# Performance work log

Hardware: AMD Instinct MI355X
Metric: run time of the kernel (lower is better)

The kernel has to match this reference:

```python
import jax, jax.numpy as jnp
import numpy as np

NUM_HEADS = 8
KERNEL = 7
LOW_RANK = 4


def setup_inputs() -> dict:
    key = jax.random.key(0)
    ks = jax.random.split(key, 10)
    B, H, W, C = 4, 56, 56, 256
    nh, K, lr = NUM_HEADS, KERNEL, LOW_RANK
    s = 0.02
    return {
        "x": jax.random.normal(ks[0], (B, H, W, C), jnp.float32),
        "Wq": jax.random.normal(ks[1], (C, nh * lr), jnp.float32) * s,
        "bq": jnp.zeros((nh * lr,), jnp.float32),
        "Wk": jax.random.normal(ks[2], (C, nh * lr), jnp.float32) * s,
        "bk": jnp.zeros((nh * lr,), jnp.float32),
        "Wv": jax.random.normal(ks[3], (C, C), jnp.float32) * s,
        "bv": jnp.zeros((C,), jnp.float32),
        "rpb": jax.random.normal(ks[4], (nh, 2 * K - 1, 2 * K - 1), jnp.float32) * s,
        "Wp": jax.random.normal(ks[5], (C, C), jnp.float32) * s,
        "bp": jnp.zeros((C,), jnp.float32),
    }


def reference(x, Wq, bq, Wk, bk, Wv, bv, rpb, Wp, bp):
    B, H, W, C = x.shape
    nh, K, lr = NUM_HEADS, KERNEL, LOW_RANK
    hd = C // nh
    r = K // 2
    scale = hd ** -0.5

    # Projections. Note: the original uses a raw reshape (B,H,W,nh*lr)->(B,nh,H,W,lr),
    # which we replicate exactly (row-major reshape, no permute).
    q = (x @ Wq + bq).reshape(B, nh, H, W, lr) * scale
    k = (x @ Wk + bk).reshape(B, nh, H, W, lr)
    v = (x @ Wv + bv).reshape(B, nh, H, W, hd)

    # NATTEN window start indices (clamped so each query sees exactly K keys per axis).
    start_h = jnp.clip(jnp.arange(H) - r, 0, H - K)  # (H,)
    start_w = jnp.clip(jnp.arange(W) - r, 0, W - K)  # (W,)
    idx_h = start_h[:, None] + jnp.arange(K)[None, :]  # (H, K)
    idx_w = start_w[:, None] + jnp.arange(K)[None, :]  # (W, K)

    # Gather local K/V windows: (B, nh, H, K, W, K, d)
    k_win = k[:, :, idx_h][:, :, :, :, idx_w]
    v_win = v[:, :, idx_h][:, :, :, :, idx_w]

    # Scores: (B, nh, H, W, K, K)
    attn = jnp.einsum('bhijc,bhikjlc->bhijkl', q, k_win)

    # Relative position bias indices: (key_pos - query_pos) + (K-1)
    bi = idx_h - jnp.arange(H)[:, None] + (K - 1)  # (H, K)
    bj = idx_w - jnp.arange(W)[:, None] + (K - 1)  # (W, K)
    bias = rpb[:, bi][:, :, :, bj]                 # (nh, H, K, W, K)
    attn = attn + bias.transpose(0, 1, 3, 2, 4)[None]  # (B, nh, H, W, K, K)

    attn = jax.nn.softmax(attn.reshape(B, nh, H, W, K * K), axis=-1)
    attn = attn.reshape(B, nh, H, W, K, K)

    # Weighted aggregation of V windows: (B, nh, H, W, hd)
    out = jnp.einsum('bhijkl,bhikjld->bhijd', attn, v_win)
    out = out.transpose(0, 2, 3, 1, 4).reshape(B, H, W, C)
    return out @ Wp + bp
```

## Files before the change

kernel.cpp:

```cpp
#include <hip/hip_runtime.h>
#include <hip/hip_bf16.h>

#define BD 4
#define HD_ 56
#define WD 56
#define CD 256
#define NH 8
#define KW 7
#define LR 4
#define HDIM 32
#define MB (HD_*WD)
#define NROWS (BD*MB)
#define QK_PER_B (HD_*WD*32)
#define V_PER_B  (HD_*WD*256)

typedef short short8 __attribute__((ext_vector_type(8)));
typedef float floatx4 __attribute__((ext_vector_type(4)));

static __device__ inline ushort f2bf(float f) {
    __hip_bfloat16 h = __float2bfloat16(f);
    return *(ushort*)&h;
}
static __device__ inline float bf2f(uint h16) {
    union { uint u; float f; } c; c.u = h16 << 16; return c.f;
}
static __device__ inline float bf2f_hi(uint u) {
    union { uint v; float f; } c; c.v = u & 0xffff0000u; return c.f;
}

typedef const __attribute__((address_space(1))) void* gp1_t;
typedef __attribute__((address_space(3))) void* sp3_t;
static __device__ __forceinline__ void glds16(const void* g, void* s) {
    __builtin_amdgcn_global_load_lds((gp1_t)g, (sp3_t)s, 16, 0, 0);
}

__global__ __launch_bounds__(256) void prep_all(
    const float* __restrict__ x,
    const float* __restrict__ Wq, const float* __restrict__ Wk,
    const float* __restrict__ Wv, const float* __restrict__ bq,
    const float* __restrict__ bk, const float* __restrict__ bv,
    const float* __restrict__ Wp,
    ushort* __restrict__ xb, ushort* __restrict__ WpkT,
    ushort* __restrict__ WpT, float* __restrict__ pb)
{
    int idx = blockIdx.x * 256 + threadIdx.x;
    if (idx < 401408) {
        float4 f0 = *(const float4*)&x[idx * 8];
        float4 f1 = *(const float4*)&x[idx * 8 + 4];
        union { ushort h[8]; uint4 u; } p;
        p.h[0] = f2bf(f0.x); p.h[1] = f2bf(f0.y); p.h[2] = f2bf(f0.z); p.h[3] = f2bf(f0.w);
        p.h[4] = f2bf(f1.x); p.h[5] = f2bf(f1.y); p.h[6] = f2bf(f1.z); p.h[7] = f2bf(f1.w);
        *(uint4*)&xb[idx * 8] = p.u;
    } else if (idx < 401408 + 81920) {
        int j = idx - 401408;
        int n = j >> 8, k = j & 255;
        float v;
        if (n < 32)       v = Wq[k * 32 + n];
        else if (n < 64)  v = Wk[k * 32 + (n - 32)];
        else              v = Wv[k * 256 + (n - 64)];
        WpkT[j] = f2bf(v);
    } else if (idx < 401408 + 81920 + 65536) {
        int j = idx - (401408 + 81920);
        int n = j >> 8, k = j & 255;
        WpT[j] = f2bf(Wp[k * 256 + n]);
    } else if (idx < 401408 + 81920 + 65536 + 320) {
        int n = idx - (401408 + 81920 + 65536);
        pb[n] = (n < 32) ? bq[n] : (n < 64) ? bk[n - 32] : bv[n - 64];
    }
}

static __device__ __forceinline__ void gemm_core_128x64(
    const ushort* __restrict__ Ag, const ushort* __restrict__ Bg,
    ushort* As, ushort* Bs, int m0, int n0, int t, floatx4 (&acc)[4][2])
{
    const int lane = t & 63, w = t >> 6;
    const int lx = lane & 7, ly = lane >> 3;
    const int koff = (lx ^ ly) << 3;
    const int col = lane & 15, quad = lane >> 4;
    const int swz = (col & 7) << 4;
    const int wm = w >> 1, wn = w & 1;
    char* Ac = (char*)As;
    char* Bc = (char*)Bs;

    for (int k0 = 0; k0 < 256; k0 += 64) {
        __syncthreads();
#pragma unroll
        for (int l = 0; l < 4; ++l) {
            int c = (w << 2) + l;
            int row = (c << 3) + ly;
            glds16(&Ag[(m0 + row) * 256 + k0 + koff], &As[c << 9]);
        }
#pragma unroll
        for (int l = 0; l < 2; ++l) {
            int c = (w << 1) + l;
            int row = (c << 3) + ly;
            glds16(&Bg[(n0 + row) * 256 + k0 + koff], &Bs[c << 9]);
        }
        __syncthreads();
#pragma unroll
        for (int kk = 0; kk < 2; ++kk) {
            const int kx = ((kk << 6) + (quad << 4)) ^ swz;
            short8 b0 = *(short8*)(Bc + ((wn << 5) + col) * 128 + kx);
            short8 b1 = *(short8*)(Bc + ((wn << 5) + 16 + col) * 128 + kx);
#pragma unroll
            for (int mt = 0; mt < 4; ++mt) {
                short8 a = *(short8*)(Ac + ((wm << 6) + (mt << 4) + col) * 128 + kx);
                acc[mt][0] = __builtin_amdgcn_mfma_f32_16x16x32_bf16(a, b0, acc[mt][0], 0, 0, 0);
                acc[mt][1] = __builtin_amdgcn_mfma_f32_16x16x32_bf16(a, b1, acc[mt][1], 0, 0, 0);
            }
        }
    }
}

__global__ __launch_bounds__(256) void mfma_qkv(
    const ushort* __restrict__ xb, const ushort* __restrict__ Bt,
    const float* __restrict__ pb, ushort* __restrict__ Qb,
    ushort* __restrict__ Kb, ushort* __restrict__ Vb)
{
    __shared__ ushort As[128 * 64];
    __shared__ ushort Bs[64 * 64];
    const int t = threadIdx.x;
    const int m0 = blockIdx.y * 128, n0 = blockIdx.x * 64;

    floatx4 acc[4][2] = {};
    gemm_core_128x64(xb, Bt, As, Bs, m0, n0, t, acc);

    const int lane = t & 63, w = t >> 6;
    const int col = lane & 15, quad = lane >> 4;
    const int wm = w >> 1, wn = w & 1;
#pragma unroll
    for (int mt = 0; mt < 4; ++mt) {
#pragma unroll
        for (int nt = 0; nt < 2; ++nt) {
            int gn = n0 + (wn << 5) + (nt << 4) + col;
            float bias = pb[gn];
#pragma unroll
            for (int rg = 0; rg < 4; ++rg) {
                int m = m0 + (wm << 6) + (mt << 4) + (quad << 2) + rg;
                ushort h = f2bf(acc[mt][nt][rg] + bias);
                if (gn < 32)        Qb[m * 32 + gn] = h;
                else if (gn < 64)   Kb[m * 32 + (gn - 32)] = h;
                else                Vb[m * 256 + (gn - 64)] = h;
            }
        }
    }
}

__global__ __launch_bounds__(256) void mfma_out(
    const ushort* __restrict__ Ag, const ushort* __restrict__ Bt,
    const float* __restrict__ bp, float* __restrict__ out)
{
    __shared__ ushort As[128 * 64];
    __shared__ ushort Bs[64 * 64];
    const int t = threadIdx.x;
    const int m0 = blockIdx.y * 128, n0 = blockIdx.x * 64;

    floatx4 acc[4][2] = {};
    gemm_core_128x64(Ag, Bt, As, Bs, m0, n0, t, acc);

    const int lane = t & 63, w = t >> 6;
    const int col = lane & 15, quad = lane >> 4;
    const int wm = w >> 1, wn = w & 1;
#pragma unroll
    for (int mt = 0; mt < 4; ++mt) {
#pragma unroll
        for (int nt = 0; nt < 2; ++nt) {
            int gn = n0 + (wn << 5) + (nt << 4) + col;
            float bias = bp[gn];
#pragma unroll
            for (int rg = 0; rg < 4; ++rg) {
                int m = m0 + (wm << 6) + (mt << 4) + (quad << 2) + rg;
                out[m * 256 + gn] = acc[mt][nt][rg] + bias;
            }
        }
    }
}

__global__ __launch_bounds__(256, 3) void natten_attn_m(
    const ushort* __restrict__ Qb, const ushort* __restrict__ Kb,
    const ushort* __restrict__ Vb, const float* __restrict__ rpb,
    ushort* __restrict__ Ab)
{
    __shared__ ushort Pl[64 * 232];
    __shared__ ushort Vt[32 * 232];
    __shared__ float4 Ksf[196];
    __shared__ float  Rs[169];
    __shared__ float  invS[64];

    const int tj = blockIdx.x, ti = blockIdx.y;
    const int n = blockIdx.z & 7, b = blockIdx.z >> 3;
    const int t = threadIdx.x;
    const int i0 = ti * 8, j0 = tj * 8;
    const int rs = min(max(i0 - 3, 0), HD_ - 14);
    const int cs = min(max(j0 - 3, 0), WD - 14);

    const ushort* kb = Kb + b * QK_PER_B + n * (HD_ * WD * LR);
    const ushort* vb = Vb + b * V_PER_B + n * (HD_ * WD * HDIM);

    uint4 vreg[4];
#pragma unroll
    for (int it = 0; it < 4; ++it) {
        int idx = t + it * 256;
        if (idx < 784) {
            int pos = idx >> 2, oct = idx & 3;
            int r = pos / 14, c = pos % 14;
            vreg[it] = *(const uint4*)&vb[(rs + r) * (WD * HDIM) + (cs + c) * HDIM + oct * 8];
        }
    }
    uint2 kreg = make_uint2(0u, 0u);
    if (t < 196) {
        int r = t / 14, c = t % 14;
        kreg = *(const uint2*)&kb[(rs + r) * (WD * LR) + (cs + c) * LR];
    }
    float rreg = (t < 169) ? rpb[n * 169 + t] : 0.f;

    const int q  = t >> 2, p = t & 3;
    const int qi = q >> 3, qj = q & 7;
    const int i = i0 + qi, j = j0 + qj;
    uint2 qr2 = *(const uint2*)&Qb[b * QK_PER_B + n * (HD_ * WD * LR) + i * (WD * LR) + j * LR];

#pragma unroll
    for (int it = 0; it < 8; ++it) {
        int idx = t + (it << 8);
        if (idx < 1856) *(uint4*)&Pl[idx << 3] = make_uint4(0, 0, 0, 0);
    }
#pragma unroll
    for (int it = 0; it < 4; ++it) {
        int idx = t + (it << 8);
        if (idx < 928) *(uint4*)&Vt[idx << 3] = make_uint4(0, 0, 0, 0);
    }
    __syncthreads();

    if (t < 196) {
        Ksf[t] = make_float4(bf2f(kreg.x & 0xffff), bf2f_hi(kreg.x),
                             bf2f(kreg.y & 0xffff), bf2f_hi(kreg.y));
    }
    if (t < 169) Rs[t] = rreg;
#pragma unroll
    for (int it = 0; it < 4; ++it) {
        int idx = t + it * 256;
        if (idx < 784) {
            int pos = idx >> 2, oct = idx & 3;
            ushort* cp = &Vt[(oct * 8) * 232 + pos];
            union { uint4 u; ushort h[8]; } vv; vv.u = vreg[it];
#pragma unroll
            for (int e = 0; e < 8; ++e) cp[e * 232] = vv.h[e];
        }
    }
    __syncthreads();

    const int sh = min(max(i - 3, 0), HD_ - KW);
    const int sw = min(max(j - 3, 0), WD - KW);
    const int oh = sh - rs, ow = sw - cs;
    const float scale = 0.17677669529663687f;
    float qx = bf2f(qr2.x & 0xffff) * scale, qy = bf2f_hi(qr2.x) * scale;
    float qz = bf2f(qr2.y & 0xffff) * scale, qw = bf2f_hi(qr2.y) * scale;
    const int rb0 = (sh - i + 6) * 13 + (sw - j + 6);

    float sum = 0.f;
#pragma unroll
    for (int half = 0; half < 2; ++half) {
        int kh = p + (half << 2);
        if (kh < 7) {
            int kpos  = (oh + kh) * 14 + ow;
            int rbase = rb0 + kh * 13;
            ushort* prow = &Pl[q * 232 + kpos];
#pragma unroll
            for (int kw = 0; kw < 7; ++kw) {
                float4 kf = Ksf[kpos + kw];
                float d = Rs[rbase + kw];
                d = fmaf(qx, kf.x, d);
                d = fmaf(qy, kf.y, d);
                d = fmaf(qz, kf.z, d);
                d = fmaf(qw, kf.w, d);
                float e = __expf(d);
                sum += e;
                prow[kw] = f2bf(e);
            }
        }
    }
    sum += __shfl_xor(sum, 1);
    sum += __shfl_xor(sum, 2);
    if (p == 0) invS[q] = 1.0f / sum;
    __syncthreads();

    const int lane = t & 63, w = t >> 6;
    const int col = lane & 15, quad = lane >> 4;
    floatx4 acc0 = {0.f, 0.f, 0.f, 0.f}, acc1 = {0.f, 0.f, 0.f, 0.f};
    const ushort* arow = &Pl[(w * 16 + col) * 232];
    const ushort* b0p  = &Vt[col * 232];
    const ushort* b1p  = &Vt[(col + 16) * 232];
#pragma unroll
    for (int s = 0; s < 7; ++s) {
        int ko = s * 32 + quad * 8;
        short8 a  = *(const short8*)(arow + ko);
        short8 f0 = *(const short8*)(b0p + ko);
        short8 f1 = *(const short8*)(b1p + ko);
        acc0 = __builtin_amdgcn_mfma_f32_16x16x32_bf16(a, f0, acc0, 0, 0, 0);
        acc1 = __builtin_amdgcn_mfma_f32_16x16x32_bf16(a, f1, acc1, 0, 0, 0);
    }

#pragma unroll
    for (int rg = 0; rg < 4; ++rg) {
        int qq = w * 16 + quad * 4 + rg;
        float iv = invS[qq];
        int ii = i0 + (qq >> 3), jj = j0 + (qq & 7);
        ushort* dst = &Ab[(((b * HD_ + ii) * WD + jj)) * CD + n * HDIM + col];
        dst[0]  = f2bf(acc0[rg] * iv);
        dst[16] = f2bf(acc1[rg] * iv);
    }
}

extern "C" void kernel_launch(void* const* d_in, const int* in_sizes, int n_in,
                              void* d_out, int out_size, void* d_ws, size_t ws_size,
                              hipStream_t stream) {
    const float* x   = (const float*)d_in[0];
    const float* Wq  = (const float*)d_in[1];
    const float* bq  = (const float*)d_in[2];
    const float* Wk  = (const float*)d_in[3];
    const float* bk  = (const float*)d_in[4];
    const float* Wv  = (const float*)d_in[5];
    const float* bv  = (const float*)d_in[6];
    const float* rpb = (const float*)d_in[7];
    const float* Wp  = (const float*)d_in[8];
    const float* bp  = (const float*)d_in[9];
    float* out = (float*)d_out;

    ushort* WpkT = (ushort*)d_ws;
    ushort* WpT  = WpkT + 81920;
    ushort* Ab   = WpT + 65536;
    ushort* Qb   = Ab + 3211264;
    ushort* Kb   = Qb + BD * QK_PER_B;
    ushort* Vb   = Kb + BD * QK_PER_B;
    ushort* xb   = Vb + BD * V_PER_B;
    float*  pb   = (float*)(xb + 3211264);

    prep_all<<<(549184 + 255) / 256, 256, 0, stream>>>(
        x, Wq, Wk, Wv, bq, bk, bv, Wp, xb, WpkT, WpT, pb);

    mfma_qkv<<<dim3(5, NROWS / 128), 256, 0, stream>>>(xb, WpkT, pb, Qb, Kb, Vb);

    natten_attn_m<<<dim3(7, 7, 32), 256, 0, stream>>>(Qb, Kb, Vb, rpb, Ab);

    mfma_out<<<dim3(4, NROWS / 128), 256, 0, stream>>>(Ab, WpT, bp, out);
}
```

Before: 114.6 us.

## Fuse neighborhood attention with output projection, looping heads per block

Merges the attention kernel and the output-projection GEMM into one kernel. Each block now handles an 8x8 spatial tile for all 8 heads, looping over heads with register prefetch of the next head's K/V/Q/rpb. The per-tile attention output stays in shared memory and is multiplied by Wp there, which removes the bf16 intermediate round-trip through global memory and one launch. In exchange the grid shrinks from 1568 to 196 blocks, so the GPU may be underfilled, and more LDS is used per block.

```diff
diff --git a/kernel.cpp b/kernel.cpp
--- a/kernel.cpp
+++ b/kernel.cpp
@@ -146,168 +146,212 @@
     }
 }
 
-__global__ __launch_bounds__(256) void mfma_out(
-    const ushort* __restrict__ Ag, const ushort* __restrict__ Bt,
-    const float* __restrict__ bp, float* __restrict__ out)
-{
-    __shared__ ushort As[128 * 64];
-    __shared__ ushort Bs[64 * 64];
-    const int t = threadIdx.x;
-    const int m0 = blockIdx.y * 128, n0 = blockIdx.x * 64;
-
-    floatx4 acc[4][2] = {};
-    gemm_core_128x64(Ag, Bt, As, Bs, m0, n0, t, acc);
-
-    const int lane = t & 63, w = t >> 6;
-    const int col = lane & 15, quad = lane >> 4;
-    const int wm = w >> 1, wn = w & 1;
-#pragma unroll
-    for (int mt = 0; mt < 4; ++mt) {
-#pragma unroll
-        for (int nt = 0; nt < 2; ++nt) {
-            int gn = n0 + (wn << 5) + (nt << 4) + col;
-            float bias = bp[gn];
-#pragma unroll
-            for (int rg = 0; rg < 4; ++rg) {
-                int m = m0 + (wm << 6) + (mt << 4) + (quad << 2) + rg;
-                out[m * 256 + gn] = acc[mt][nt][rg] + bias;
-            }
-        }
-    }
-}
-
-__global__ __launch_bounds__(256, 3) void natten_attn_m(
+__global__ __launch_bounds__(256) void natten_fused(
     const ushort* __restrict__ Qb, const ushort* __restrict__ Kb,
     const ushort* __restrict__ Vb, const float* __restrict__ rpb,
-    ushort* __restrict__ Ab)
+    const ushort* __restrict__ WpT, const float* __restrict__ bp,
+    float* __restrict__ out)
 {
-    __shared__ ushort Pl[64 * 232];
-    __shared__ ushort Vt[32 * 232];
-    __shared__ float4 Ksf[196];
-    __shared__ float  Rs[169];
-    __shared__ float  invS[64];
-
-    const int tj = blockIdx.x, ti = blockIdx.y;
-    const int n = blockIdx.z & 7, b = blockIdx.z >> 3;
+    __shared__ __align__(16) ushort Olds[64 * 264];
+    __shared__ __align__(16) ushort Vt[32 * 232];
+    __shared__ __align__(16) char   Preg[33792];
+    ushort* Pl   = (ushort*)Preg;
+    float4* Ksf  = (float4*)(Preg + 29696);
+    float*  Rs   = (float*)(Preg + 32832);
+    float*  invS = (float*)(Preg + 33512);
+    ushort* Bsg  = (ushort*)Preg;
+
+    const int tj = blockIdx.x, ti = blockIdx.y, b = blockIdx.z;
     const int t = threadIdx.x;
     const int i0 = ti * 8, j0 = tj * 8;
     const int rs = min(max(i0 - 3, 0), HD_ - 14);
     const int cs = min(max(j0 - 3, 0), WD - 14);
 
-    const ushort* kb = Kb + b * QK_PER_B + n * (HD_ * WD * LR);
-    const ushort* vb = Vb + b * V_PER_B + n * (HD_ * WD * HDIM);
-
-    uint4 vreg[4];
-#pragma unroll
-    for (int it = 0; it < 4; ++it) {
-        int idx = t + it * 256;
-        if (idx < 784) {
-            int pos = idx >> 2, oct = idx & 3;
-            int r = pos / 14, c = pos % 14;
-            vreg[it] = *(const uint4*)&vb[(rs + r) * (WD * HDIM) + (cs + c) * HDIM + oct * 8];
-        }
-    }
-    uint2 kreg = make_uint2(0u, 0u);
-    if (t < 196) {
-        int r = t / 14, c = t % 14;
-        kreg = *(const uint2*)&kb[(rs + r) * (WD * LR) + (cs + c) * LR];
-    }
-    float rreg = (t < 169) ? rpb[n * 169 + t] : 0.f;
-
     const int q  = t >> 2, p = t & 3;
     const int qi = q >> 3, qj = q & 7;
     const int i = i0 + qi, j = j0 + qj;
-    uint2 qr2 = *(const uint2*)&Qb[b * QK_PER_B + n * (HD_ * WD * LR) + i * (WD * LR) + j * LR];
+    const int lane = t & 63, w = t >> 6;
+    const int col = lane & 15, quad = lane >> 4;
+
+    const int sh = min(max(i - 3, 0), HD_ - KW);
+    const int sw = min(max(j - 3, 0), WD - KW);
+    const int oh = sh - rs, ow = sw - cs;
+    const int rb0 = (sh - i + 6) * 13 + (sw - j + 6);
+    const float scale = 0.17677669529663687f;
 
 #pragma unroll
     for (int it = 0; it < 8; ++it) {
         int idx = t + (it << 8);
-        if (idx < 1856) *(uint4*)&Pl[idx << 3] = make_uint4(0, 0, 0, 0);
+        if (idx < 1856) *(uint4*)&Preg[idx << 4] = make_uint4(0, 0, 0, 0);
     }
 #pragma unroll
     for (int it = 0; it < 4; ++it) {
         int idx = t + (it << 8);
         if (idx < 928) *(uint4*)&Vt[idx << 3] = make_uint4(0, 0, 0, 0);
     }
+
+    uint4 vreg[4];
+    uint2 kreg = make_uint2(0u, 0u), qcur, qnext;
+    float rreg = 0.f;
+    {
+        const ushort* vb = Vb + (size_t)b * V_PER_B;
+        const ushort* kb = Kb + (size_t)b * QK_PER_B;
+#pragma unroll
+        for (int it = 0; it < 4; ++it) {
+            int idx = t + it * 256;
+            if (idx < 784) {
+                int pos = idx >> 2, oct = idx & 3;
+                int r = pos / 14, c = pos % 14;
+                vreg[it] = *(const uint4*)&vb[(rs + r) * (WD * HDIM) + (cs + c) * HDIM + oct * 8];
+            }
+        }
+        if (t < 196) {
+            int r = t / 14, c = t % 14;
+            kreg = *(const uint2*)&kb[(rs + r) * (WD * LR) + (cs + c) * LR];
+        }
+        if (t < 169) rreg = rpb[t];
+        qcur = *(const uint2*)&Qb[(size_t)b * QK_PER_B + i * (WD * LR) + j * LR];
+    }
     __syncthreads();
 
-    if (t < 196) {
-        Ksf[t] = make_float4(bf2f(kreg.x & 0xffff), bf2f_hi(kreg.x),
-                             bf2f(kreg.y & 0xffff), bf2f_hi(kreg.y));
-    }
-    if (t < 169) Rs[t] = rreg;
-#pragma unroll
-    for (int it = 0; it < 4; ++it) {
-        int idx = t + it * 256;
-        if (idx < 784) {
-            int pos = idx >> 2, oct = idx & 3;
-            ushort* cp = &Vt[(oct * 8) * 232 + pos];
-            union { uint4 u; ushort h[8]; } vv; vv.u = vreg[it];
-#pragma unroll
-            for (int e = 0; e < 8; ++e) cp[e * 232] = vv.h[e];
-        }
-    }
-    __syncthreads();
-
-    const int sh = min(max(i - 3, 0), HD_ - KW);
-    const int sw = min(max(j - 3, 0), WD - KW);
-    const int oh = sh - rs, ow = sw - cs;
-    const float scale = 0.17677669529663687f;
-    float qx = bf2f(qr2.x & 0xffff) * scale, qy = bf2f_hi(qr2.x) * scale;
-    float qz = bf2f(qr2.y & 0xffff) * scale, qw = bf2f_hi(qr2.y) * scale;
-    const int rb0 = (sh - i + 6) * 13 + (sw - j + 6);
-
-    float sum = 0.f;
-#pragma unroll
-    for (int half = 0; half < 2; ++half) {
-        int kh = p + (half << 2);
-        if (kh < 7) {
-            int kpos  = (oh + kh) * 14 + ow;
-            int rbase = rb0 + kh * 13;
-            ushort* prow = &Pl[q * 232 + kpos];
-#pragma unroll
-            for (int kw = 0; kw < 7; ++kw) {
-                float4 kf = Ksf[kpos + kw];
-                float d = Rs[rbase + kw];
-                d = fmaf(qx, kf.x, d);
-                d = fmaf(qy, kf.y, d);
-                d = fmaf(qz, kf.z, d);
-                d = fmaf(qw, kf.w, d);
-                float e = __expf(d);
-                sum += e;
-                prow[kw] = f2bf(e);
-            }
-        }
-    }
-    sum += __shfl_xor(sum, 1);
-    sum += __shfl_xor(sum, 2);
-    if (p == 0) invS[q] = 1.0f / sum;
-    __syncthreads();
-
-    const int lane = t & 63, w = t >> 6;
-    const int col = lane & 15, quad = lane >> 4;
-    floatx4 acc0 = {0.f, 0.f, 0.f, 0.f}, acc1 = {0.f, 0.f, 0.f, 0.f};
-    const ushort* arow = &Pl[(w * 16 + col) * 232];
-    const ushort* b0p  = &Vt[col * 232];
-    const ushort* b1p  = &Vt[(col + 16) * 232];
-#pragma unroll
-    for (int s = 0; s < 7; ++s) {
-        int ko = s * 32 + quad * 8;
-        short8 a  = *(const short8*)(arow + ko);
-        short8 f0 = *(const short8*)(b0p + ko);
-        short8 f1 = *(const short8*)(b1p + ko);
-        acc0 = __builtin_amdgcn_mfma_f32_16x16x32_bf16(a, f0, acc0, 0, 0, 0);
-        acc1 = __builtin_amdgcn_mfma_f32_16x16x32_bf16(a, f1, acc1, 0, 0, 0);
-    }
-
-#pragma unroll
-    for (int rg = 0; rg < 4; ++rg) {
-        int qq = w * 16 + quad * 4 + rg;
-        float iv = invS[qq];
-        int ii = i0 + (qq >> 3), jj = j0 + (qq & 7);
-        ushort* dst = &Ab[(((b * HD_ + ii) * WD + jj)) * CD + n * HDIM + col];
-        dst[0]  = f2bf(acc0[rg] * iv);
-        dst[16] = f2bf(acc1[rg] * iv);
+    for (int h = 0; h < 8; ++h) {
+#pragma unroll
+        for (int it = 0; it < 4; ++it) {
+            int idx = t + it * 256;
+            if (idx < 784) {
+                int pos = idx >> 2, oct = idx & 3;
+                ushort* cp = &Vt[(oct * 8) * 232 + pos];
+                union { uint4 u; ushort hh[8]; } vv; vv.u = vreg[it];
+#pragma unroll
+                for (int e = 0; e < 8; ++e) cp[e * 232] = vv.hh[e];
+            }
+        }
+        if (t < 196) {
+            Ksf[t] = make_float4(bf2f(kreg.x & 0xffff), bf2f_hi(kreg.x),
+                                 bf2f(kreg.y & 0xffff), bf2f_hi(kreg.y));
+        }
+        if (t < 169) Rs[t] = rreg;
+        __syncthreads();
+
+        if (h < 7) {
+            const ushort* vb = Vb + (size_t)b * V_PER_B + (h + 1) * (HD_ * WD * HDIM);
+            const ushort* kb = Kb + (size_t)b * QK_PER_B + (h + 1) * (HD_ * WD * LR);
+#pragma unroll
+            for (int it = 0; it < 4; ++it) {
+                int idx = t + it * 256;
+                if (idx < 784) {
+                    int pos = idx >> 2, oct = idx & 3;
+                    int r = pos / 14, c = pos % 14;
+                    vreg[it] = *(const uint4*)&vb[(rs + r) * (WD * HDIM) + (cs + c) * HDIM + oct * 8];
+                }
+            }
+            if (t < 196) {
+                int r = t / 14, c = t % 14;
+                kreg = *(const uint2*)&kb[(rs + r) * (WD * LR) + (cs + c) * LR];
+            }
+            if (t < 169) rreg = rpb[(h + 1) * 169 + t];
+            qnext = *(const uint2*)&Qb[(size_t)b * QK_PER_B + (h + 1) * (HD_ * WD * LR) + i * (WD * LR) + j * LR];
+        }
+
+        float qx = bf2f(qcur.x & 0xffff) * scale, qy = bf2f_hi(qcur.x) * scale;
+        float qz = bf2f(qcur.y & 0xffff) * scale, qw = bf2f_hi(qcur.y) * scale;
+        float sum = 0.f;
+#pragma unroll
+        for (int half = 0; half < 2; ++half) {
+            int kh = p + (half << 2);
+            if (kh < 7) {
+                int kpos  = (oh + kh) * 14 + ow;
+                int rbase = rb0 + kh * 13;
+                ushort* prow = &Pl[q * 232 + kpos];
+#pragma unroll
+                for (int kw = 0; kw < 7; ++kw) {
+                    float4 kf = Ksf[kpos + kw];
+                    float d = Rs[rbase + kw];
+                    d = fmaf(qx, kf.x, d);
+                    d = fmaf(qy, kf.y, d);
+                    d = fmaf(qz, kf.z, d);
+                    d = fmaf(qw, kf.w, d);
+                    float e = __expf(d);
+                    sum += e;
+                    prow[kw] = f2bf(e);
+                }
+            }
+        }
+        sum += __shfl_xor(sum, 1);
+        sum += __shfl_xor(sum, 2);
+        if (p == 0) invS[q] = 1.0f / sum;
+        __syncthreads();
+
+        floatx4 acc0 = {0.f, 0.f, 0.f, 0.f}, acc1 = {0.f, 0.f, 0.f, 0.f};
+        const ushort* arow = &Pl[(w * 16 + col) * 232];
+        const ushort* b0p  = &Vt[col * 232];
+        const ushort* b1p  = &Vt[(col + 16) * 232];
+#pragma unroll
+        for (int s = 0; s < 7; ++s) {
+            int ko = s * 32 + quad * 8;
+            short8 a  = *(const short8*)(arow + ko);
+            short8 f0 = *(const short8*)(b0p + ko);
+            short8 f1 = *(const short8*)(b1p + ko);
+            acc0 = __builtin_amdgcn_mfma_f32_16x16x32_bf16(a, f0, acc0, 0, 0, 0);
+            acc1 = __builtin_amdgcn_mfma_f32_16x16x32_bf16(a, f1, acc1, 0, 0, 0);
+        }
+
+#pragma unroll
+        for (int rg = 0; rg < 4; ++rg) {
+            int qq = w * 16 + quad * 4 + rg;
+            float iv = invS[qq];
+            Olds[qq * 264 + h * 32 + col]      = f2bf(acc0[rg] * iv);
+            Olds[qq * 264 + h * 32 + col + 16] = f2bf(acc1[rg] * iv);
+        }
+        qcur = qnext;
+        __syncthreads();
+    }
+
+    const int lx = lane & 7, ly = lane >> 3;
+    const int koff = (lx ^ ly) << 3;
+    const int swz = (col & 7) << 4;
+    char* Bc = (char*)Bsg;
+    floatx4 acc[4][4] = {};
+
+    for (int k0 = 0; k0 < 256; k0 += 64) {
+        __syncthreads();
+#pragma unroll
+        for (int l = 0; l < 8; ++l) {
+            int c = (w << 3) + l;
+            int row = (c << 3) + ly;
+            glds16(&WpT[row * 256 + k0 + koff], &Bsg[c << 9]);
+        }
+        __syncthreads();
+#pragma unroll
+        for (int kk = 0; kk < 2; ++kk) {
+            const int kx = ((kk << 6) + (quad << 4)) ^ swz;
+            short8 bf[4];
+#pragma unroll
+            for (int nt = 0; nt < 4; ++nt)
+                bf[nt] = *(short8*)(Bc + ((w << 6) + (nt << 4) + col) * 128 + kx);
+#pragma unroll
+            for (int mt = 0; mt < 4; ++mt) {
+                short8 a = *(const short8*)&Olds[((mt << 4) + col) * 264 + k0 + (kk << 5) + (quad << 3)];
+#pragma unroll
+                for (int nt = 0; nt < 4; ++nt)
+                    acc[mt][nt] = __builtin_amdgcn_mfma_f32_16x16x32_bf16(a, bf[nt], acc[mt][nt], 0, 0, 0);
+            }
+        }
+    }
+
+#pragma unroll
+    for (int mt = 0; mt < 4; ++mt) {
+#pragma unroll
+        for (int rg = 0; rg < 4; ++rg) {
+            int qq = (mt << 4) + (quad << 2) + rg;
+            int ii = i0 + (qq >> 3), jj = j0 + (qq & 7);
+            float* orow = &out[(((b * HD_ + ii) * WD + jj)) * CD];
+#pragma unroll
+            for (int nt = 0; nt < 4; ++nt) {
+                int gn = (w << 6) + (nt << 4) + col;
+                orow[gn] = acc[mt][nt][rg] + bp[gn];
+            }
+        }
     }
 }
 
@@ -328,8 +372,7 @@
 
     ushort* WpkT = (ushort*)d_ws;
     ushort* WpT  = WpkT + 81920;
-    ushort* Ab   = WpT + 65536;
-    ushort* Qb   = Ab + 3211264;
+    ushort* Qb   = WpT + 65536;
     ushort* Kb   = Qb + BD * QK_PER_B;
     ushort* Vb   = Kb + BD * QK_PER_B;
     ushort* xb   = Vb + BD * V_PER_B;
@@ -340,7 +383,5 @@
 
     mfma_qkv<<<dim3(5, NROWS / 128), 256, 0, stream>>>(xb, WpkT, pb, Qb, Kb, Vb);
 
-    natten_attn_m<<<dim3(7, 7, 32), 256, 0, stream>>>(Qb, Kb, Vb, rpb, Ab);
-
-    mfma_out<<<dim3(4, NROWS / 128), 256, 0, stream>>>(Ab, WpT, bp, out);
-}
+    natten_fused<<<dim3(7, 7, BD), 256, 0, stream>>>(Qb, Kb, Vb, rpb, WpT, bp, out);
+}
```

New measurement: 127.0 us. +10.9%, slower.

## Shrink attention and output GEMM tiles for more blocks and occupancy

Applied to the files above, without the earlier changes.

The attention kernel now handles 4x8 query tiles per block instead of 8x8, with 8 threads per query (one per window row), smaller LDS buffers, and one MFMA accumulator per wave over 5 K-steps. Launch bounds rise to allow 6 blocks per CU. The output projection GEMM drops from 128x64 to 64x64 tiles, using an inline swizzled LDS load loop, which doubles the grid. The aim is more parallelism and better latency hiding, at the cost of more redundant halo loads of K and V per query and less reuse per GEMM tile.

```diff
diff --git a/kernel.cpp b/kernel.cpp
--- a/kernel.cpp
+++ b/kernel.cpp
@@ -146,168 +146,173 @@
     }
 }
 
-__global__ __launch_bounds__(256) void mfma_out(
+__global__ __launch_bounds__(256, 6) void natten_attn4(
+    const ushort* __restrict__ Qb, const ushort* __restrict__ Kb,
+    const ushort* __restrict__ Vb, const float* __restrict__ rpb,
+    ushort* __restrict__ Ab)
+{
+    __shared__ __align__(16) ushort Pl[32 * 168];
+    __shared__ __align__(16) ushort Vt[32 * 168];
+    __shared__ float4 Ksf[140];
+    __shared__ float  Rs[169];
+    __shared__ float  invS[32];
+
+    const int tj = blockIdx.x, ti = blockIdx.y;
+    const int h = blockIdx.z & 7, b = blockIdx.z >> 3;
+    const int t = threadIdx.x;
+    const int i0 = ti * 4, j0 = tj * 8;
+    const int rs = min(max(i0 - 3, 0), HD_ - 10);
+    const int cs = min(max(j0 - 3, 0), WD - 14);
+
+    const ushort* kb = Kb + (size_t)b * QK_PER_B + h * (HD_ * WD * LR);
+    const ushort* vb = Vb + (size_t)b * V_PER_B + h * (HD_ * WD * HDIM);
+
+#pragma unroll
+    for (int it = 0; it < 3; ++it) {
+        int idx = t + (it << 8);
+        if (idx < 672) {
+            *(uint4*)&Pl[idx << 3] = make_uint4(0, 0, 0, 0);
+            *(uint4*)&Vt[idx << 3] = make_uint4(0, 0, 0, 0);
+        }
+    }
+    __syncthreads();
+
+    if (t < 140) {
+        int r = t / 14, c = t % 14;
+        uint2 kr = *(const uint2*)&kb[(rs + r) * (WD * LR) + (cs + c) * LR];
+        Ksf[t] = make_float4(bf2f(kr.x & 0xffff), bf2f_hi(kr.x),
+                             bf2f(kr.y & 0xffff), bf2f_hi(kr.y));
+    }
+    if (t < 169) Rs[t] = rpb[h * 169 + t];
+#pragma unroll
+    for (int it = 0; it < 3; ++it) {
+        int idx = t + (it << 8);
+        if (idx < 560) {
+            int oct = idx / 140, pos = idx % 140;
+            int r = pos / 14, c = pos % 14;
+            union { uint4 u; ushort hh[8]; } vv;
+            vv.u = *(const uint4*)&vb[(rs + r) * (WD * HDIM) + (cs + c) * HDIM + oct * 8];
+            ushort* cp = &Vt[(oct * 8) * 168 + pos];
+#pragma unroll
+            for (int e = 0; e < 8; ++e) cp[e * 168] = vv.hh[e];
+        }
+    }
+
+    const int q  = t >> 3, p = t & 7;
+    const int qi = q >> 3, qj = q & 7;
+    const int i = i0 + qi, j = j0 + qj;
+    uint2 qr2 = *(const uint2*)&Qb[(size_t)b * QK_PER_B + h * (HD_ * WD * LR) + i * (WD * LR) + j * LR];
+    __syncthreads();
+
+    const int sh = min(max(i - 3, 0), HD_ - KW);
+    const int sw = min(max(j - 3, 0), WD - KW);
+    const int oh = sh - rs, ow = sw - cs;
+    const int rb0 = (sh - i + 6) * 13 + (sw - j + 6);
+    const float scale = 0.17677669529663687f;
+    float qx = bf2f(qr2.x & 0xffff) * scale, qy = bf2f_hi(qr2.x) * scale;
+    float qz = bf2f(qr2.y & 0xffff) * scale, qw = bf2f_hi(qr2.y) * scale;
+
+    float sum = 0.f;
+    if (p < 7) {
+        int kpos  = (oh + p) * 14 + ow;
+        int rbase = rb0 + p * 13;
+        ushort* prow = &Pl[q * 168 + kpos];
+#pragma unroll
+        for (int kw = 0; kw < 7; ++kw) {
+            float4 kf = Ksf[kpos + kw];
+            float d = Rs[rbase + kw];
+            d = fmaf(qx, kf.x, d);
+            d = fmaf(qy, kf.y, d);
+            d = fmaf(qz, kf.z, d);
+            d = fmaf(qw, kf.w, d);
+            float e = __expf(d);
+            sum += e;
+            prow[kw] = f2bf(e);
+        }
+    }
+    sum += __shfl_xor(sum, 1);
+    sum += __shfl_xor(sum, 2);
+    sum += __shfl_xor(sum, 4);
+    if (p == 0) invS[q] = 1.0f / sum;
+    __syncthreads();
+
+    const int lane = t & 63, w = t >> 6;
+    const int col = lane & 15, quad = lane >> 4;
+    const int wm = w & 1, wn = w >> 1;
+    floatx4 acc = {0.f, 0.f, 0.f, 0.f};
+    const ushort* arow = &Pl[(wm * 16 + col) * 168];
+    const ushort* brow = &Vt[(wn * 16 + col) * 168];
+#pragma unroll
+    for (int s = 0; s < 5; ++s) {
+        int ko = s * 32 + quad * 8;
+        short8 a  = *(const short8*)(arow + ko);
+        short8 bb = *(const short8*)(brow + ko);
+        acc = __builtin_amdgcn_mfma_f32_16x16x32_bf16(a, bb, acc, 0, 0, 0);
+    }
+
+#pragma unroll
+    for (int rg = 0; rg < 4; ++rg) {
+        int qq = wm * 16 + quad * 4 + rg;
+        float iv = invS[qq];
+        int ii = i0 + (qq >> 3), jj = j0 + (qq & 7);
+        Ab[(((b * HD_ + ii) * WD + jj)) * CD + h * HDIM + wn * 16 + col] = f2bf(acc[rg] * iv);
+    }
+}
+
+__global__ __launch_bounds__(256) void mfma_out64(
     const ushort* __restrict__ Ag, const ushort* __restrict__ Bt,
     const float* __restrict__ bp, float* __restrict__ out)
 {
-    __shared__ ushort As[128 * 64];
+    __shared__ ushort As[64 * 64];
     __shared__ ushort Bs[64 * 64];
     const int t = threadIdx.x;
-    const int m0 = blockIdx.y * 128, n0 = blockIdx.x * 64;
-
-    floatx4 acc[4][2] = {};
-    gemm_core_128x64(Ag, Bt, As, Bs, m0, n0, t, acc);
-
+    const int m0 = blockIdx.y * 64, n0 = blockIdx.x * 64;
     const int lane = t & 63, w = t >> 6;
+    const int lx = lane & 7, ly = lane >> 3;
+    const int koff = (lx ^ ly) << 3;
     const int col = lane & 15, quad = lane >> 4;
+    const int swz = (col & 7) << 4;
     const int wm = w >> 1, wn = w & 1;
-#pragma unroll
-    for (int mt = 0; mt < 4; ++mt) {
+    char* Ac = (char*)As;
+    char* Bc = (char*)Bs;
+    floatx4 acc[2][2] = {};
+
+    for (int k0 = 0; k0 < 256; k0 += 64) {
+        __syncthreads();
+#pragma unroll
+        for (int l = 0; l < 2; ++l) {
+            int c = (w << 1) + l;
+            int row = (c << 3) + ly;
+            glds16(&Ag[(m0 + row) * 256 + k0 + koff], &As[c << 9]);
+            glds16(&Bt[(n0 + row) * 256 + k0 + koff], &Bs[c << 9]);
+        }
+        __syncthreads();
+#pragma unroll
+        for (int kk = 0; kk < 2; ++kk) {
+            const int kx = ((kk << 6) + (quad << 4)) ^ swz;
+            short8 b0 = *(short8*)(Bc + ((wn << 5) + col) * 128 + kx);
+            short8 b1 = *(short8*)(Bc + ((wn << 5) + 16 + col) * 128 + kx);
+#pragma unroll
+            for (int mt = 0; mt < 2; ++mt) {
+                short8 a = *(short8*)(Ac + ((wm << 5) + (mt << 4) + col) * 128 + kx);
+                acc[mt][0] = __builtin_amdgcn_mfma_f32_16x16x32_bf16(a, b0, acc[mt][0], 0, 0, 0);
+                acc[mt][1] = __builtin_amdgcn_mfma_f32_16x16x32_bf16(a, b1, acc[mt][1], 0, 0, 0);
+            }
+        }
+    }
+
+#pragma unroll
+    for (int mt = 0; mt < 2; ++mt) {
 #pragma unroll
         for (int nt = 0; nt < 2; ++nt) {
             int gn = n0 + (wn << 5) + (nt << 4) + col;
             float bias = bp[gn];
 #pragma unroll
             for (int rg = 0; rg < 4; ++rg) {
-                int m = m0 + (wm << 6) + (mt << 4) + (quad << 2) + rg;
+                int m = m0 + (wm << 5) + (mt << 4) + (quad << 2) + rg;
                 out[m * 256 + gn] = acc[mt][nt][rg] + bias;
             }
         }
-    }
-}
-
-__global__ __launch_bounds__(256, 3) void natten_attn_m(
-    const ushort* __restrict__ Qb, const ushort* __restrict__ Kb,
-    const ushort* __restrict__ Vb, const float* __restrict__ rpb,
-    ushort* __restrict__ Ab)
-{
-    __shared__ ushort Pl[64 * 232];
-    __shared__ ushort Vt[32 * 232];
-    __shared__ float4 Ksf[196];
-    __shared__ float  Rs[169];
-    __shared__ float  invS[64];
-
-    const int tj = blockIdx.x, ti = blockIdx.y;
-    const int n = blockIdx.z & 7, b = blockIdx.z >> 3;
-    const int t = threadIdx.x;
-    const int i0 = ti * 8, j0 = tj * 8;
-    const int rs = min(max(i0 - 3, 0), HD_ - 14);
-    const int cs = min(max(j0 - 3, 0), WD - 14);
-
-    const ushort* kb = Kb + b * QK_PER_B + n * (HD_ * WD * LR);
-    const ushort* vb = Vb + b * V_PER_B + n * (HD_ * WD * HDIM);
-
-    uint4 vreg[4];
-#pragma unroll
-    for (int it = 0; it < 4; ++it) {
-        int idx = t + it * 256;
-        if (idx < 784) {
-            int pos = idx >> 2, oct = idx & 3;
-            int r = pos / 14, c = pos % 14;
-            vreg[it] = *(const uint4*)&vb[(rs + r) * (WD * HDIM) + (cs + c) * HDIM + oct * 8];
-        }
-    }
-    uint2 kreg = make_uint2(0u, 0u);
-    if (t < 196) {
-        int r = t / 14, c = t % 14;
-        kreg = *(const uint2*)&kb[(rs + r) * (WD * LR) + (cs + c) * LR];
-    }
-    float rreg = (t < 169) ? rpb[n * 169 + t] : 0.f;
-
-    const int q  = t >> 2, p = t & 3;
-    const int qi = q >> 3, qj = q & 7;
-    const int i = i0 + qi, j = j0 + qj;
-    uint2 qr2 = *(const uint2*)&Qb[b * QK_PER_B + n * (HD_ * WD * LR) + i * (WD * LR) + j * LR];
-
-#pragma unroll
-    for (int it = 0; it < 8; ++it) {
-        int idx = t + (it << 8);
-        if (idx < 1856) *(uint4*)&Pl[idx << 3] = make_uint4(0, 0, 0, 0);
-    }
-#pragma unroll
-    for (int it = 0; it < 4; ++it) {
-        int idx = t + (it << 8);
-        if (idx < 928) *(uint4*)&Vt[idx << 3] = make_uint4(0, 0, 0, 0);
-    }
-    __syncthreads();
-
-    if (t < 196) {
-        Ksf[t] = make_float4(bf2f(kreg.x & 0xffff), bf2f_hi(kreg.x),
-                             bf2f(kreg.y & 0xffff), bf2f_hi(kreg.y));
-    }
-    if (t < 169) Rs[t] = rreg;
-#pragma unroll
-    for (int it = 0; it < 4; ++it) {
-        int idx = t + it * 256;
-        if (idx < 784) {
-            int pos = idx >> 2, oct = idx & 3;
-            ushort* cp = &Vt[(oct * 8) * 232 + pos];
-            union { uint4 u; ushort h[8]; } vv; vv.u = vreg[it];
-#pragma unroll
-            for (int e = 0; e < 8; ++e) cp[e * 232] = vv.h[e];
-        }
-    }
-    __syncthreads();
-
-    const int sh = min(max(i - 3, 0), HD_ - KW);
-    const int sw = min(max(j - 3, 0), WD - KW);
-    const int oh = sh - rs, ow = sw - cs;
-    const float scale = 0.17677669529663687f;
-    float qx = bf2f(qr2.x & 0xffff) * scale, qy = bf2f_hi(qr2.x) * scale;
-    float qz = bf2f(qr2.y & 0xffff) * scale, qw = bf2f_hi(qr2.y) * scale;
-    const int rb0 = (sh - i + 6) * 13 + (sw - j + 6);
-
-    float sum = 0.f;
-#pragma unroll
-    for (int half = 0; half < 2; ++half) {
-        int kh = p + (half << 2);
-        if (kh < 7) {
-            int kpos  = (oh + kh) * 14 + ow;
-            int rbase = rb0 + kh * 13;
-            ushort* prow = &Pl[q * 232 + kpos];
-#pragma unroll
-            for (int kw = 0; kw < 7; ++kw) {
-                float4 kf = Ksf[kpos + kw];
-                float d = Rs[rbase + kw];
-                d = fmaf(qx, kf.x, d);
-                d = fmaf(qy, kf.y, d);
-                d = fmaf(qz, kf.z, d);
-                d = fmaf(qw, kf.w, d);
-                float e = __expf(d);
-                sum += e;
-                prow[kw] = f2bf(e);
-            }
-        }
-    }
-    sum += __shfl_xor(sum, 1);
-    sum += __shfl_xor(sum, 2);
-    if (p == 0) invS[q] = 1.0f / sum;
-    __syncthreads();
-
-    const int lane = t & 63, w = t >> 6;
-    const int col = lane & 15, quad = lane >> 4;
-    floatx4 acc0 = {0.f, 0.f, 0.f, 0.f}, acc1 = {0.f, 0.f, 0.f, 0.f};
-    const ushort* arow = &Pl[(w * 16 + col) * 232];
-    const ushort* b0p  = &Vt[col * 232];
-    const ushort* b1p  = &Vt[(col + 16) * 232];
-#pragma unroll
-    for (int s = 0; s < 7; ++s) {
-        int ko = s * 32 + quad * 8;
-        short8 a  = *(const short8*)(arow + ko);
-        short8 f0 = *(const short8*)(b0p + ko);
-        short8 f1 = *(const short8*)(b1p + ko);
-        acc0 = __builtin_amdgcn_mfma_f32_16x16x32_bf16(a, f0, acc0, 0, 0, 0);
-        acc1 = __builtin_amdgcn_mfma_f32_16x16x32_bf16(a, f1, acc1, 0, 0, 0);
-    }
-
-#pragma unroll
-    for (int rg = 0; rg < 4; ++rg) {
-        int qq = w * 16 + quad * 4 + rg;
-        float iv = invS[qq];
-        int ii = i0 + (qq >> 3), jj = j0 + (qq & 7);
-        ushort* dst = &Ab[(((b * HD_ + ii) * WD + jj)) * CD + n * HDIM + col];
-        dst[0]  = f2bf(acc0[rg] * iv);
-        dst[16] = f2bf(acc1[rg] * iv);
     }
 }
 
@@ -340,7 +345,7 @@
 
     mfma_qkv<<<dim3(5, NROWS / 128), 256, 0, stream>>>(xb, WpkT, pb, Qb, Kb, Vb);
 
-    natten_attn_m<<<dim3(7, 7, 32), 256, 0, stream>>>(Qb, Kb, Vb, rpb, Ab);
-
-    mfma_out<<<dim3(4, NROWS / 128), 256, 0, stream>>>(Ab, WpT, bp, out);
-}
+    natten_attn4<<<dim3(7, 14, 32), 256, 0, stream>>>(Qb, Kb, Vb, rpb, Ab);
+
+    mfma_out64<<<dim3(4, 196), 256, 0, stream>>>(Ab, WpT, bp, out);
+}
```

Measured after the change: 112.2 us. -2.1%, faster.
